# Kernel optimization log

Measured on AMD Instinct MI355X. Metric: run time of the kernel, lower is better.

## Reference

```python
import jax, jax.numpy as jnp
import numpy as np

LENGTHSCALE = 1.0


def setup_inputs() -> dict:
    key = jax.random.key(0)
    k1, k2, k3 = jax.random.split(key, 3)
    M, N, D = 4096, 8192, 256
    X = jax.random.normal(k1, (M, D), dtype=jnp.float32)
    X_train = jax.random.normal(k2, (N, D), dtype=jnp.float32)
    alpha = jax.random.normal(k3, (N, 1), dtype=jnp.float32)
    return {"X": X, "X_train": X_train, "alpha": alpha}


def _rbf_kernel(X1, X2, lengthscale=LENGTHSCALE):
    # Same math as sum((X1[:,None]-X2[None,:])**2, -1) without the [M,N,D] tensor.
    sq1 = jnp.sum(X1 * X1, axis=-1, keepdims=True)          # [M,1]
    sq2 = jnp.sum(X2 * X2, axis=-1)                         # [N]
    dist_sq = sq1 + sq2[None, :] - 2.0 * (X1 @ X2.T)        # [M,N]
    return jnp.exp(-dist_sq / (2.0 * lengthscale ** 2))


def reference(X, X_train, alpha):
    K_star = _rbf_kernel(X, X_train)    # [M,N]
    pred = K_star @ alpha               # [M,1]
    return pred
```

## Files before the change

kernel.cpp:

```cpp
#include <hip/hip_runtime.h>
#include <hip/hip_bf16.h>

#define M_DIM 4096
#define N_DIM 8192
#define D_DIM 256
#define NSLICE 32
#define C_EXP (-0.7213475204444817f)
#define K_ACC (1.4426950408889634f)
#define SKIP_THR (-151.0f)

#define AS1 __attribute__((address_space(1)))
#define AS3 __attribute__((address_space(3)))

typedef __attribute__((ext_vector_type(8))) short short8;
typedef __attribute__((ext_vector_type(4))) float f32x4;

__device__ inline unsigned short f2bf(float f) {
    __hip_bfloat16 h = __float2bfloat16(f);
    return *reinterpret_cast<unsigned short*>(&h);
}

__global__ __launch_bounds__(256) void prep_kernel(
    const float* __restrict__ X, const float* __restrict__ T,
    const float* __restrict__ alpha,
    unsigned short* __restrict__ Xb, unsigned short* __restrict__ Tb,
    float* __restrict__ sq1, float2* __restrict__ sqal)
{
    const int row  = blockIdx.x * 4 + (threadIdx.x >> 6);
    const int lane = threadIdx.x & 63;
    const float* src; char* dstB; int r, nrows; bool isX;
    if (row < M_DIM) { src = X; dstB = (char*)Xb; r = row; nrows = M_DIM; isX = true; }
    else { src = T; dstB = (char*)Tb; r = row - M_DIM; nrows = N_DIM; isX = false; }

    const float4* s4 = reinterpret_cast<const float4*>(src + (size_t)r * D_DIM);
    float4 v = s4[lane];
    float ss = v.x * v.x + v.y * v.y + v.z * v.z + v.w * v.w;

    ushort4 b4;
    b4.x = f2bf(v.x); b4.y = f2bf(v.y); b4.z = f2bf(v.z); b4.w = f2bf(v.w);
    const int gslot = lane >> 1;
    const int kt    = gslot >> 3;
    const int ss16  = (gslot & 7) ^ (r & 7);
    *reinterpret_cast<ushort4*>(dstB +
        ((size_t)kt * nrows + r) * 128 + ss16 * 16 + (lane & 1) * 8) = b4;

    #pragma unroll
    for (int o = 1; o < 64; o <<= 1) ss += __shfl_xor(ss, o);
    if (lane == 0) {
        if (isX) sq1[r] = ss * C_EXP;
        else     sqal[r] = make_float2(ss * C_EXP, alpha[r]);
    }
}

__global__ __launch_bounds__(512, 2) void gemm_kernel(
    const unsigned short* __restrict__ Xb, const unsigned short* __restrict__ Tb,
    const float* __restrict__ sq1, const float2* __restrict__ sqal,
    float* __restrict__ part)
{
    __shared__ __align__(16) char smem[131072];
    const int g    = blockIdx.x >> 6;
    const int r    = blockIdx.x & 63;
    const int bn   = g * 4 + (r & 3);
    const int bm   = r >> 2;
    const int tid  = threadIdx.x;
    const int wid  = tid >> 6;
    const int lane = tid & 63;
    const int l15  = lane & 15, lg = lane >> 4, xr = l15 & 7;
    const int wr   = wid >> 2, wc = wid & 3;
    const char* XbB = (const char*)Xb;
    const char* TbB = (const char*)Tb;

    auto stage_op = [&](int ktn, int h, int blk) {
        const int dest = (ktn & 1) * 65536 + (h & 1) * 32768
                       + (h >> 1) * 16384 + blk * 1024;
        const char* sb = (h < 2) ? XbB : TbB;
        const int nrows = (h < 2) ? M_DIM : N_DIM;
        const int rc0 = ((h < 2) ? bm : bn) * 256 + (h & 1) * 128 + blk * 8;
        const size_t src = ((size_t)ktn * nrows + rc0) * 128 + (size_t)lane * 16;
        __builtin_amdgcn_global_load_lds(
            (const AS1 void*)(sb + src), (AS3 void*)(smem + dest), 16, 0, 0);
    };
    auto stageP0 = [&](int ktn) {
        #pragma unroll
        for (int c = 0; c < 4; ++c) {
            const int o = wid * 4 + c;
            int h, blk;
            if (o < 16) { h = o >> 3; blk = o & 7; }
            else { const int s = o & 15; h = 2 + (s >> 3);
                   const int bb = s & 7; blk = (bb & 3) + ((bb >> 2) << 3); }
            stage_op(ktn, h, blk);
        }
    };
    auto stageP1 = [&](int ktn) {
        #pragma unroll
        for (int c = 0; c < 2; ++c) {
            const int o = wid * 2 + c;
            const int bb = o & 7;
            stage_op(ktn, 2 + (o >> 3), 4 + (bb & 3) + ((bb >> 2) << 3));
        }
    };
    auto stageP2 = [&](int ktn) {
        #pragma unroll
        for (int c = 0; c < 2; ++c) {
            const int o = wid * 2 + c;
            stage_op(ktn, o >> 3, 8 + (o & 7));
        }
    };

    f32x4 acc[8][4];
    #pragma unroll
    for (int m = 0; m < 8; ++m)
        #pragma unroll
        for (int n = 0; n < 4; ++n) acc[m][n] = (f32x4)0.0f;

    stageP0(0); stageP1(0); stageP2(0);

    short8 af0[4][2], af1[4][2], bf0[2][2], bf1[2][2];

    #pragma unroll
    for (int kt = 0; kt < 4; ++kt) {
        const char* Abase = smem + (kt & 1) * 65536 + wr * 32768;
        const char* Bbase = smem + (kt & 1) * 65536 + 16384 + (wc >> 1) * 32768
                          + (wc & 1) * 8192;

        if (kt < 3) { stageP0(kt + 1);
                      asm volatile("s_waitcnt vmcnt(8)" ::: "memory"); }
        else          asm volatile("s_waitcnt vmcnt(4)" ::: "memory");
        asm volatile("s_barrier" ::: "memory");
        #pragma unroll
        for (int m = 0; m < 4; ++m)
            #pragma unroll
            for (int ks = 0; ks < 2; ++ks)
                af0[m][ks] = *(const short8*)(Abase + (m * 16 + l15) * 128
                                              + (((ks * 4 + lg) ^ xr)) * 16);
        #pragma unroll
        for (int n = 0; n < 2; ++n)
            #pragma unroll
            for (int ks = 0; ks < 2; ++ks)
                bf0[n][ks] = *(const short8*)(Bbase + (n * 16 + l15) * 128
                                              + (((ks * 4 + lg) ^ xr)) * 16);
        __builtin_amdgcn_s_setprio(1);
        #pragma unroll
        for (int ks = 0; ks < 2; ++ks)
            #pragma unroll
            for (int m = 0; m < 4; ++m)
                #pragma unroll
                for (int n = 0; n < 2; ++n)
                    acc[m][n] = __builtin_amdgcn_mfma_f32_16x16x32_bf16(
                        af0[m][ks], bf0[n][ks], acc[m][n], 0, 0, 0);
        __builtin_amdgcn_s_setprio(0);

        if (kt < 3) { stageP1(kt + 1);
                      asm volatile("s_waitcnt vmcnt(8)" ::: "memory"); }
        else          asm volatile("s_waitcnt vmcnt(2)" ::: "memory");
        asm volatile("s_barrier" ::: "memory");
        #pragma unroll
        for (int n = 0; n < 2; ++n)
            #pragma unroll
            for (int ks = 0; ks < 2; ++ks)
                bf1[n][ks] = *(const short8*)(Bbase + (32 + n * 16 + l15) * 128
                                              + (((ks * 4 + lg) ^ xr)) * 16);
        __builtin_amdgcn_s_setprio(1);
        #pragma unroll
        for (int ks = 0; ks < 2; ++ks)
            #pragma unroll
            for (int m = 0; m < 4; ++m)
                #pragma unroll
                for (int n = 0; n < 2; ++n)
                    acc[m][2 + n] = __builtin_amdgcn_mfma_f32_16x16x32_bf16(
                        af0[m][ks], bf1[n][ks], acc[m][2 + n], 0, 0, 0);
        __builtin_amdgcn_s_setprio(0);

        if (kt < 3) { stageP2(kt + 1);
                      asm volatile("s_waitcnt vmcnt(8)" ::: "memory"); }
        else          asm volatile("s_waitcnt vmcnt(0)" ::: "memory");
        asm volatile("s_barrier" ::: "memory");
        #pragma unroll
        for (int m = 0; m < 4; ++m)
            #pragma unroll
            for (int ks = 0; ks < 2; ++ks)
                af1[m][ks] = *(const short8*)(Abase + (64 + m * 16 + l15) * 128
                                              + (((ks * 4 + lg) ^ xr)) * 16);
        __builtin_amdgcn_s_setprio(1);
        #pragma unroll
        for (int ks = 0; ks < 2; ++ks)
            #pragma unroll
            for (int m = 0; m < 4; ++m)
                #pragma unroll
                for (int n = 0; n < 2; ++n)
                    acc[4 + m][2 + n] = __builtin_amdgcn_mfma_f32_16x16x32_bf16(
                        af1[m][ks], bf1[n][ks], acc[4 + m][2 + n], 0, 0, 0);
        __builtin_amdgcn_s_setprio(0);

        __builtin_amdgcn_s_setprio(1);
        #pragma unroll
        for (int ks = 0; ks < 2; ++ks)
            #pragma unroll
            for (int m = 0; m < 4; ++m)
                #pragma unroll
                for (int n = 0; n < 2; ++n)
                    acc[4 + m][n] = __builtin_amdgcn_mfma_f32_16x16x32_bf16(
                        af1[m][ks], bf0[n][ks], acc[4 + m][n], 0, 0, 0);
        __builtin_amdgcn_s_setprio(0);
    }

    const int rowbase = bm * 256 + wr * 128;
    float4 s1v[8];
    #pragma unroll
    for (int m = 0; m < 8; ++m)
        s1v[m] = *reinterpret_cast<const float4*>(sq1 + rowbase + m * 16 + lg * 4);
    float2 sa[4];
    #pragma unroll
    for (int n = 0; n < 4; ++n)
        sa[n] = sqal[bn * 256 + wc * 64 + n * 16 + l15];

    float amax = acc[0][0][0], s1m = s1v[0][0], s2m = sa[0].x;
    #pragma unroll
    for (int m = 0; m < 8; ++m)
        #pragma unroll
        for (int n = 0; n < 4; ++n)
            #pragma unroll
            for (int rr = 0; rr < 4; ++rr) amax = fmaxf(amax, acc[m][n][rr]);
    #pragma unroll
    for (int m = 0; m < 8; ++m)
        #pragma unroll
        for (int rr = 0; rr < 4; ++rr) s1m = fmaxf(s1m, s1v[m][rr]);
    #pragma unroll
    for (int n = 0; n < 4; ++n) s2m = fmaxf(s2m, sa[n].x);

    float psum[8][4];
    #pragma unroll
    for (int m = 0; m < 8; ++m)
        #pragma unroll
        for (int rr = 0; rr < 4; ++rr) psum[m][rr] = 0.0f;

    const float bound = fmaf(amax, K_ACC, s1m + s2m);
    if (!__all(bound < SKIP_THR)) {
        #pragma unroll
        for (int m = 0; m < 8; ++m)
            #pragma unroll
            for (int n = 0; n < 4; ++n)
                #pragma unroll
                for (int rr = 0; rr < 4; ++rr) {
                    const float arg = fmaf(acc[m][n][rr], K_ACC, s1v[m][rr] + sa[n].x);
                    psum[m][rr] = fmaf(__builtin_amdgcn_exp2f(arg), sa[n].y, psum[m][rr]);
                }
    }

    float* red = (float*)smem;
    #pragma unroll
    for (int m = 0; m < 8; ++m) {
        float4 pv;
        #pragma unroll
        for (int rr = 0; rr < 4; ++rr) {
            float p = psum[m][rr];
            p += __shfl_xor(p, 1);
            p += __shfl_xor(p, 2);
            p += __shfl_xor(p, 4);
            p += __shfl_xor(p, 8);
            ((float*)&pv)[rr] = p;
        }
        if (l15 == 0)
            *reinterpret_cast<float4*>(&red[wc * 256 + wr * 128 + m * 16 + lg * 4]) = pv;
    }
    __syncthreads();
    if (tid < 256) {
        const float s = red[tid] + red[256 + tid] + red[512 + tid] + red[768 + tid];
        part[(size_t)bn * M_DIM + bm * 256 + tid] = s;
    }
}

__global__ __launch_bounds__(256) void reduce_kernel(
    const float* __restrict__ part, float* __restrict__ out)
{
    const int gi = blockIdx.x * 256 + threadIdx.x;
    float s = 0.0f;
    #pragma unroll
    for (int b = 0; b < NSLICE; ++b) s += part[(size_t)b * M_DIM + gi];
    out[gi] = s;
}

extern "C" void kernel_launch(void* const* d_in, const int* in_sizes, int n_in,
                              void* d_out, int out_size, void* d_ws, size_t ws_size,
                              hipStream_t stream)
{
    const float* X  = (const float*)d_in[0];
    const float* T  = (const float*)d_in[1];
    const float* al = (const float*)d_in[2];
    float* out = (float*)d_out;

    char* ws = (char*)d_ws;
    unsigned short* Xb = (unsigned short*)ws;
    unsigned short* Tb = (unsigned short*)(ws + (size_t)M_DIM * D_DIM * 2);
    float* sq1  = (float*)(ws + (size_t)(M_DIM + N_DIM) * D_DIM * 2);
    float2* sqal = (float2*)(sq1 + M_DIM);
    float* part = (float*)(sqal + N_DIM);

    prep_kernel<<<(M_DIM + N_DIM) / 4, 256, 0, stream>>>(X, T, al, Xb, Tb, sq1, sqal);
    gemm_kernel<<<(M_DIM / 256) * NSLICE, 512, 0, stream>>>(Xb, Tb, sq1, sqal, part);
    reduce_kernel<<<M_DIM / 256, 256, 0, stream>>>(part, out);
}
```

Baseline: 36.09 us.

## Process two N-tiles per block with cross-tile prefetch and drop LDS reduction

Each GEMM block now computes two adjacent 256-column tiles in sequence, continuing the double-buffered load pipeline across the tile boundary so the next tile's loads overlap the current epilogue. The grid shrinks to one block per tile pair. The in-block LDS cross-wave reduction and barrier are removed; each wave column writes its own partial row sums to global memory, and the reduce kernel now sums 128 slices instead of 32. This trades a larger partial buffer and a heavier final reduction for fewer block launches and better overlap.

```diff
diff --git a/kernel.cpp b/kernel.cpp
--- a/kernel.cpp
+++ b/kernel.cpp
@@ -4,7 +4,6 @@
 #define M_DIM 4096
 #define N_DIM 8192
 #define D_DIM 256
-#define NSLICE 32
 #define C_EXP (-0.7213475204444817f)
 #define K_ACC (1.4426950408889634f)
 #define SKIP_THR (-151.0f)
@@ -55,13 +54,12 @@
 __global__ __launch_bounds__(512, 2) void gemm_kernel(
     const unsigned short* __restrict__ Xb, const unsigned short* __restrict__ Tb,
     const float* __restrict__ sq1, const float2* __restrict__ sqal,
-    float* __restrict__ part)
+    float* __restrict__ part2)
 {
     __shared__ __align__(16) char smem[131072];
-    const int g    = blockIdx.x >> 6;
-    const int r    = blockIdx.x & 63;
-    const int bn   = g * 4 + (r & 3);
-    const int bm   = r >> 2;
+    const int t    = blockIdx.x;
+    const int bm   = t >> 4;
+    const int bn2  = t & 15;
     const int tid  = threadIdx.x;
     const int wid  = tid >> 6;
     const int lane = tid & 63;
@@ -70,17 +68,20 @@
     const char* XbB = (const char*)Xb;
     const char* TbB = (const char*)Tb;
 
-    auto stage_op = [&](int ktn, int h, int blk) {
-        const int dest = (ktn & 1) * 65536 + (h & 1) * 32768
+    auto stage_op = [&](int Kn, int h, int blk) {
+        const int dest = (Kn & 1) * 65536 + (h & 1) * 32768
                        + (h >> 1) * 16384 + blk * 1024;
         const char* sb = (h < 2) ? XbB : TbB;
         const int nrows = (h < 2) ? M_DIM : N_DIM;
-        const int rc0 = ((h < 2) ? bm : bn) * 256 + (h & 1) * 128 + blk * 8;
-        const size_t src = ((size_t)ktn * nrows + rc0) * 128 + (size_t)lane * 16;
+        const int base = (h < 2) ? bm : (bn2 * 2 + (Kn >> 2));
+        const int rc0 = base * 256 + (h & 1) * 128 + blk * 8;
+        const size_t src = ((size_t)(Kn & 3) * nrows + rc0) * 128
+                         + (size_t)lane * 16;
         __builtin_amdgcn_global_load_lds(
             (const AS1 void*)(sb + src), (AS3 void*)(smem + dest), 16, 0, 0);
     };
-    auto stageP0 = [&](int ktn) {
+    auto stageP0 = [&](int Kn) {
+        if (Kn > 7) return;
         #pragma unroll
         for (int c = 0; c < 4; ++c) {
             const int o = wid * 4 + c;
@@ -88,195 +89,199 @@
             if (o < 16) { h = o >> 3; blk = o & 7; }
             else { const int s = o & 15; h = 2 + (s >> 3);
                    const int bb = s & 7; blk = (bb & 3) + ((bb >> 2) << 3); }
-            stage_op(ktn, h, blk);
+            stage_op(Kn, h, blk);
         }
     };
-    auto stageP1 = [&](int ktn) {
+    auto stageP1 = [&](int Kn) {
+        if (Kn > 7) return;
         #pragma unroll
         for (int c = 0; c < 2; ++c) {
             const int o = wid * 2 + c;
             const int bb = o & 7;
-            stage_op(ktn, 2 + (o >> 3), 4 + (bb & 3) + ((bb >> 2) << 3));
+            stage_op(Kn, 2 + (o >> 3), 4 + (bb & 3) + ((bb >> 2) << 3));
         }
     };
-    auto stageP2 = [&](int ktn) {
+    auto stageP2 = [&](int Kn) {
+        if (Kn > 7) return;
         #pragma unroll
         for (int c = 0; c < 2; ++c) {
             const int o = wid * 2 + c;
-            stage_op(ktn, o >> 3, 8 + (o & 7));
+            stage_op(Kn, o >> 3, 8 + (o & 7));
         }
     };
 
-    f32x4 acc[8][4];
-    #pragma unroll
-    for (int m = 0; m < 8; ++m)
-        #pragma unroll
-        for (int n = 0; n < 4; ++n) acc[m][n] = (f32x4)0.0f;
-
     stageP0(0); stageP1(0); stageP2(0);
 
     short8 af0[4][2], af1[4][2], bf0[2][2], bf1[2][2];
 
-    #pragma unroll
-    for (int kt = 0; kt < 4; ++kt) {
-        const char* Abase = smem + (kt & 1) * 65536 + wr * 32768;
-        const char* Bbase = smem + (kt & 1) * 65536 + 16384 + (wc >> 1) * 32768
-                          + (wc & 1) * 8192;
-
-        if (kt < 3) { stageP0(kt + 1);
-                      asm volatile("s_waitcnt vmcnt(8)" ::: "memory"); }
-        else          asm volatile("s_waitcnt vmcnt(4)" ::: "memory");
-        asm volatile("s_barrier" ::: "memory");
-        #pragma unroll
-        for (int m = 0; m < 4; ++m)
+    #pragma unroll 1
+    for (int job = 0; job < 2; ++job) {
+        f32x4 acc[8][4];
+        #pragma unroll
+        for (int m = 0; m < 8; ++m)
+            #pragma unroll
+            for (int n = 0; n < 4; ++n) acc[m][n] = (f32x4)0.0f;
+
+        #pragma unroll
+        for (int kt = 0; kt < 4; ++kt) {
+            const int K = job * 4 + kt;
+            const char* Abase = smem + (K & 1) * 65536 + wr * 32768;
+            const char* Bbase = smem + (K & 1) * 65536 + 16384
+                              + (wc >> 1) * 32768 + (wc & 1) * 8192;
+
+            if (K < 7) { stageP0(K + 1);
+                         asm volatile("s_waitcnt vmcnt(8)" ::: "memory"); }
+            else         asm volatile("s_waitcnt vmcnt(4)" ::: "memory");
+            asm volatile("s_barrier" ::: "memory");
+            #pragma unroll
+            for (int m = 0; m < 4; ++m)
+                #pragma unroll
+                for (int ks = 0; ks < 2; ++ks)
+                    af0[m][ks] = *(const short8*)(Abase + (m * 16 + l15) * 128
+                                                  + (((ks * 4 + lg) ^ xr)) * 16);
+            #pragma unroll
+            for (int n = 0; n < 2; ++n)
+                #pragma unroll
+                for (int ks = 0; ks < 2; ++ks)
+                    bf0[n][ks] = *(const short8*)(Bbase + (n * 16 + l15) * 128
+                                                  + (((ks * 4 + lg) ^ xr)) * 16);
+            __builtin_amdgcn_s_setprio(1);
             #pragma unroll
             for (int ks = 0; ks < 2; ++ks)
-                af0[m][ks] = *(const short8*)(Abase + (m * 16 + l15) * 128
-                                              + (((ks * 4 + lg) ^ xr)) * 16);
-        #pragma unroll
-        for (int n = 0; n < 2; ++n)
+                #pragma unroll
+                for (int m = 0; m < 4; ++m)
+                    #pragma unroll
+                    for (int n = 0; n < 2; ++n)
+                        acc[m][n] = __builtin_amdgcn_mfma_f32_16x16x32_bf16(
+                            af0[m][ks], bf0[n][ks], acc[m][n], 0, 0, 0);
+            __builtin_amdgcn_s_setprio(0);
+
+            if (K < 7) { stageP1(K + 1);
+                         asm volatile("s_waitcnt vmcnt(8)" ::: "memory"); }
+            else         asm volatile("s_waitcnt vmcnt(2)" ::: "memory");
+            asm volatile("s_barrier" ::: "memory");
+            #pragma unroll
+            for (int n = 0; n < 2; ++n)
+                #pragma unroll
+                for (int ks = 0; ks < 2; ++ks)
+                    bf1[n][ks] = *(const short8*)(Bbase + (32 + n * 16 + l15) * 128
+                                                  + (((ks * 4 + lg) ^ xr)) * 16);
+            __builtin_amdgcn_s_setprio(1);
             #pragma unroll
             for (int ks = 0; ks < 2; ++ks)
-                bf0[n][ks] = *(const short8*)(Bbase + (n * 16 + l15) * 128
-                                              + (((ks * 4 + lg) ^ xr)) * 16);
-        __builtin_amdgcn_s_setprio(1);
-        #pragma unroll
-        for (int ks = 0; ks < 2; ++ks)
+                #pragma unroll
+                for (int m = 0; m < 4; ++m)
+                    #pragma unroll
+                    for (int n = 0; n < 2; ++n)
+                        acc[m][2 + n] = __builtin_amdgcn_mfma_f32_16x16x32_bf16(
+                            af0[m][ks], bf1[n][ks], acc[m][2 + n], 0, 0, 0);
+            __builtin_amdgcn_s_setprio(0);
+
+            if (K < 7) { stageP2(K + 1);
+                         asm volatile("s_waitcnt vmcnt(8)" ::: "memory"); }
+            else         asm volatile("s_waitcnt vmcnt(0)" ::: "memory");
+            asm volatile("s_barrier" ::: "memory");
             #pragma unroll
             for (int m = 0; m < 4; ++m)
                 #pragma unroll
-                for (int n = 0; n < 2; ++n)
-                    acc[m][n] = __builtin_amdgcn_mfma_f32_16x16x32_bf16(
-                        af0[m][ks], bf0[n][ks], acc[m][n], 0, 0, 0);
-        __builtin_amdgcn_s_setprio(0);
-
-        if (kt < 3) { stageP1(kt + 1);
-                      asm volatile("s_waitcnt vmcnt(8)" ::: "memory"); }
-        else          asm volatile("s_waitcnt vmcnt(2)" ::: "memory");
-        asm volatile("s_barrier" ::: "memory");
-        #pragma unroll
-        for (int n = 0; n < 2; ++n)
+                for (int ks = 0; ks < 2; ++ks)
+                    af1[m][ks] = *(const short8*)(Abase + (64 + m * 16 + l15) * 128
+                                                  + (((ks * 4 + lg) ^ xr)) * 16);
+            __builtin_amdgcn_s_setprio(1);
             #pragma unroll
             for (int ks = 0; ks < 2; ++ks)
-                bf1[n][ks] = *(const short8*)(Bbase + (32 + n * 16 + l15) * 128
-                                              + (((ks * 4 + lg) ^ xr)) * 16);
-        __builtin_amdgcn_s_setprio(1);
-        #pragma unroll
-        for (int ks = 0; ks < 2; ++ks)
-            #pragma unroll
-            for (int m = 0; m < 4; ++m)
-                #pragma unroll
-                for (int n = 0; n < 2; ++n)
-                    acc[m][2 + n] = __builtin_amdgcn_mfma_f32_16x16x32_bf16(
-                        af0[m][ks], bf1[n][ks], acc[m][2 + n], 0, 0, 0);
-        __builtin_amdgcn_s_setprio(0);
-
-        if (kt < 3) { stageP2(kt + 1);
-                      asm volatile("s_waitcnt vmcnt(8)" ::: "memory"); }
-        else          asm volatile("s_waitcnt vmcnt(0)" ::: "memory");
-        asm volatile("s_barrier" ::: "memory");
-        #pragma unroll
-        for (int m = 0; m < 4; ++m)
+                #pragma unroll
+                for (int m = 0; m < 4; ++m)
+                    #pragma unroll
+                    for (int n = 0; n < 2; ++n)
+                        acc[4 + m][2 + n] = __builtin_amdgcn_mfma_f32_16x16x32_bf16(
+                            af1[m][ks], bf1[n][ks], acc[4 + m][2 + n], 0, 0, 0);
+            __builtin_amdgcn_s_setprio(0);
+
+            __builtin_amdgcn_s_setprio(1);
             #pragma unroll
             for (int ks = 0; ks < 2; ++ks)
-                af1[m][ks] = *(const short8*)(Abase + (64 + m * 16 + l15) * 128
-                                              + (((ks * 4 + lg) ^ xr)) * 16);
-        __builtin_amdgcn_s_setprio(1);
-        #pragma unroll
-        for (int ks = 0; ks < 2; ++ks)
-            #pragma unroll
-            for (int m = 0; m < 4; ++m)
-                #pragma unroll
-                for (int n = 0; n < 2; ++n)
-                    acc[4 + m][2 + n] = __builtin_amdgcn_mfma_f32_16x16x32_bf16(
-                        af1[m][ks], bf1[n][ks], acc[4 + m][2 + n], 0, 0, 0);
-        __builtin_amdgcn_s_setprio(0);
-
-        __builtin_amdgcn_s_setprio(1);
-        #pragma unroll
-        for (int ks = 0; ks < 2; ++ks)
-            #pragma unroll
-            for (int m = 0; m < 4; ++m)
-                #pragma unroll
-                for (int n = 0; n < 2; ++n)
-                    acc[4 + m][n] = __builtin_amdgcn_mfma_f32_16x16x32_bf16(
-                        af1[m][ks], bf0[n][ks], acc[4 + m][n], 0, 0, 0);
-        __builtin_amdgcn_s_setprio(0);
+                #pragma unroll
+                for (int m = 0; m < 4; ++m)
+                    #pragma unroll
+                    for (int n = 0; n < 2; ++n)
+                        acc[4 + m][n] = __builtin_amdgcn_mfma_f32_16x16x32_bf16(
+                            af1[m][ks], bf0[n][ks], acc[4 + m][n], 0, 0, 0);
+            __builtin_amdgcn_s_setprio(0);
+        }
+
+        const int bnJ = bn2 * 2 + job;
+        const int rowbase = bm * 256 + wr * 128;
+        float4 s1v[8];
+        #pragma unroll
+        for (int m = 0; m < 8; ++m)
+            s1v[m] = *reinterpret_cast<const float4*>(sq1 + rowbase + m * 16 + lg * 4);
+        float2 sa[4];
+        #pragma unroll
+        for (int n = 0; n < 4; ++n)
+            sa[n] = sqal[bnJ * 256 + wc * 64 + n * 16 + l15];
+
+        float amax = acc[0][0][0], s1m = s1v[0][0], s2m = sa[0].x;
+        #pragma unroll
+        for (int m = 0; m < 8; ++m)
+            #pragma unroll
+            for (int n = 0; n < 4; ++n)
+                #pragma unroll
+                for (int rr = 0; rr < 4; ++rr) amax = fmaxf(amax, acc[m][n][rr]);
+        #pragma unroll
+        for (int m = 0; m < 8; ++m)
+            #pragma unroll
+            for (int rr = 0; rr < 4; ++rr) s1m = fmaxf(s1m, s1v[m][rr]);
+        #pragma unroll
+        for (int n = 0; n < 4; ++n) s2m = fmaxf(s2m, sa[n].x);
+
+        float psum[8][4];
+        #pragma unroll
+        for (int m = 0; m < 8; ++m)
+            #pragma unroll
+            for (int rr = 0; rr < 4; ++rr) psum[m][rr] = 0.0f;
+
+        const float bound = fmaf(amax, K_ACC, s1m + s2m);
+        if (!__all(bound < SKIP_THR)) {
+            #pragma unroll
+            for (int m = 0; m < 8; ++m)
+                #pragma unroll
+                for (int n = 0; n < 4; ++n)
+                    #pragma unroll
+                    for (int rr = 0; rr < 4; ++rr) {
+                        const float arg = fmaf(acc[m][n][rr], K_ACC,
+                                               s1v[m][rr] + sa[n].x);
+                        psum[m][rr] = fmaf(__builtin_amdgcn_exp2f(arg),
+                                           sa[n].y, psum[m][rr]);
+                    }
+        }
+
+        float* dst = part2 + ((size_t)(bnJ * 4 + wc)) * M_DIM + rowbase;
+        #pragma unroll
+        for (int m = 0; m < 8; ++m) {
+            float4 pv;
+            #pragma unroll
+            for (int rr = 0; rr < 4; ++rr) {
+                float p = psum[m][rr];
+                p += __shfl_xor(p, 1);
+                p += __shfl_xor(p, 2);
+                p += __shfl_xor(p, 4);
+                p += __shfl_xor(p, 8);
+                ((float*)&pv)[rr] = p;
+            }
+            if (l15 == 0)
+                *reinterpret_cast<float4*>(dst + m * 16 + lg * 4) = pv;
+        }
     }
-
-    const int rowbase = bm * 256 + wr * 128;
-    float4 s1v[8];
-    #pragma unroll
-    for (int m = 0; m < 8; ++m)
-        s1v[m] = *reinterpret_cast<const float4*>(sq1 + rowbase + m * 16 + lg * 4);
-    float2 sa[4];
-    #pragma unroll
-    for (int n = 0; n < 4; ++n)
-        sa[n] = sqal[bn * 256 + wc * 64 + n * 16 + l15];
-
-    float amax = acc[0][0][0], s1m = s1v[0][0], s2m = sa[0].x;
-    #pragma unroll
-    for (int m = 0; m < 8; ++m)
-        #pragma unroll
-        for (int n = 0; n < 4; ++n)
-            #pragma unroll
-            for (int rr = 0; rr < 4; ++rr) amax = fmaxf(amax, acc[m][n][rr]);
-    #pragma unroll
-    for (int m = 0; m < 8; ++m)
-        #pragma unroll
-        for (int rr = 0; rr < 4; ++rr) s1m = fmaxf(s1m, s1v[m][rr]);
-    #pragma unroll
-    for (int n = 0; n < 4; ++n) s2m = fmaxf(s2m, sa[n].x);
-
-    float psum[8][4];
-    #pragma unroll
-    for (int m = 0; m < 8; ++m)
-        #pragma unroll
-        for (int rr = 0; rr < 4; ++rr) psum[m][rr] = 0.0f;
-
-    const float bound = fmaf(amax, K_ACC, s1m + s2m);
-    if (!__all(bound < SKIP_THR)) {
-        #pragma unroll
-        for (int m = 0; m < 8; ++m)
-            #pragma unroll
-            for (int n = 0; n < 4; ++n)
-                #pragma unroll
-                for (int rr = 0; rr < 4; ++rr) {
-                    const float arg = fmaf(acc[m][n][rr], K_ACC, s1v[m][rr] + sa[n].x);
-                    psum[m][rr] = fmaf(__builtin_amdgcn_exp2f(arg), sa[n].y, psum[m][rr]);
-                }
-    }
-
-    float* red = (float*)smem;
-    #pragma unroll
-    for (int m = 0; m < 8; ++m) {
-        float4 pv;
-        #pragma unroll
-        for (int rr = 0; rr < 4; ++rr) {
-            float p = psum[m][rr];
-            p += __shfl_xor(p, 1);
-            p += __shfl_xor(p, 2);
-            p += __shfl_xor(p, 4);
-            p += __shfl_xor(p, 8);
-            ((float*)&pv)[rr] = p;
-        }
-        if (l15 == 0)
-            *reinterpret_cast<float4*>(&red[wc * 256 + wr * 128 + m * 16 + lg * 4]) = pv;
-    }
-    __syncthreads();
-    if (tid < 256) {
-        const float s = red[tid] + red[256 + tid] + red[512 + tid] + red[768 + tid];
-        part[(size_t)bn * M_DIM + bm * 256 + tid] = s;
-    }
 }
 
 __global__ __launch_bounds__(256) void reduce_kernel(
-    const float* __restrict__ part, float* __restrict__ out)
+    const float* __restrict__ part2, float* __restrict__ out)
 {
     const int gi = blockIdx.x * 256 + threadIdx.x;
     float s = 0.0f;
-    #pragma unroll
-    for (int b = 0; b < NSLICE; ++b) s += part[(size_t)b * M_DIM + gi];
+    #pragma unroll 8
+    for (int b = 0; b < 128; ++b) s += part2[(size_t)b * M_DIM + gi];
     out[gi] = s;
 }
 
@@ -294,9 +299,9 @@
     unsigned short* Tb = (unsigned short*)(ws + (size_t)M_DIM * D_DIM * 2);
     float* sq1  = (float*)(ws + (size_t)(M_DIM + N_DIM) * D_DIM * 2);
     float2* sqal = (float2*)(sq1 + M_DIM);
-    float* part = (float*)(sqal + N_DIM);
+    float* part2 = (float*)(sqal + N_DIM);
 
     prep_kernel<<<(M_DIM + N_DIM) / 4, 256, 0, stream>>>(X, T, al, Xb, Tb, sq1, sqal);
-    gemm_kernel<<<(M_DIM / 256) * NSLICE, 512, 0, stream>>>(Xb, Tb, sq1, sqal, part);
-    reduce_kernel<<<M_DIM / 256, 256, 0, stream>>>(part, out);
-}
+    gemm_kernel<<<256, 512, 0, stream>>>(Xb, Tb, sq1, sqal, part2);
+    reduce_kernel<<<M_DIM / 256, 256, 0, stream>>>(part2, out);
+}
```

Result: slower. 53.07 us (+47.1%).
